# Performance work log

Hardware: AMD Instinct MI355X
Metric: run time of the kernel (lower is better)

## Reference

```python
import jax, jax.numpy as jnp
import numpy as np

N_NODES = 50000
N_EDGES = 800000
IN_DIM = 512
HEADS = 4
HID = 64
OUT = 64
NEG_SLOPE = 0.2  # DGL GATConv default


def gat_layer(x, W, attn_l, attn_r, bias, src, dst, n_nodes, heads, d_out):
    # x: [N, F_in], W: [F_in, heads*d_out], attn_l/attn_r: [heads, d_out], bias: [heads, d_out]
    f = (x @ W).reshape(n_nodes, heads, d_out)          # [N, H, D]
    el = jnp.sum(f * attn_l, axis=-1)                   # [N, H]
    er = jnp.sum(f * attn_r, axis=-1)                   # [N, H]
    e = jax.nn.leaky_relu(el[src] + er[dst], NEG_SLOPE) # [E, H]
    # segment softmax over incoming edges of each dst node
    m = jax.ops.segment_max(e, dst, num_segments=n_nodes)       # [N, H]
    ex = jnp.exp(e - m[dst])                                     # [E, H]
    den = jax.ops.segment_sum(ex, dst, num_segments=n_nodes)    # [N, H]
    a = ex / den[dst]                                            # [E, H]
    # scatter-aggregate weighted messages
    out = jax.ops.segment_sum(a[:, :, None] * f[src], dst, num_segments=n_nodes)  # [N, H, D]
    return out + bias, a


def setup_inputs() -> dict:
    key = jax.random.key(0)
    ks = jax.random.split(key, 12)
    features = jax.random.normal(ks[0], (N_NODES, IN_DIM), dtype=jnp.float32)
    src = jax.random.randint(ks[1], (N_EDGES,), 0, N_NODES, dtype=jnp.int32)
    dst = jax.random.randint(ks[2], (N_EDGES,), 0, N_NODES, dtype=jnp.int32)
    s1 = 1.0 / np.sqrt(IN_DIM)
    s2 = 1.0 / np.sqrt(HEADS * HID)
    W1 = jax.random.normal(ks[3], (IN_DIM, HEADS * HID), dtype=jnp.float32) * s1
    al1 = jax.random.normal(ks[4], (HEADS, HID), dtype=jnp.float32) * s1
    ar1 = jax.random.normal(ks[5], (HEADS, HID), dtype=jnp.float32) * s1
    b1 = jnp.zeros((HEADS, HID), dtype=jnp.float32)
    W2 = jax.random.normal(ks[6], (HEADS * HID, OUT), dtype=jnp.float32) * s2
    al2 = jax.random.normal(ks[7], (1, OUT), dtype=jnp.float32) * s2
    ar2 = jax.random.normal(ks[8], (1, OUT), dtype=jnp.float32) * s2
    b2 = jnp.zeros((1, OUT), dtype=jnp.float32)
    return {"features": features, "W1": W1, "al1": al1, "ar1": ar1, "b1": b1,
            "W2": W2, "al2": al2, "ar2": ar2, "b2": b2, "src": src, "dst": dst}


def reference(features, W1, al1, ar1, b1, W2, al2, ar2, b2, src, dst):
    h1, _ = gat_layer(features, W1, al1, ar1, b1, src, dst, N_NODES, HEADS, HID)
    h1 = jax.nn.elu(h1.reshape(N_NODES, HEADS * HID))   # flatten heads + ELU
    h2, _ = gat_layer(h1, W2, al2, ar2, b2, src, dst, N_NODES, 1, OUT)
    return h2  # [N, 1, OUT]
```

## Files before the change

kernel.cpp:

```cpp
#include <hip/hip_runtime.h>

#define N_NODES 50000
#define N_EDGES 800000
#define IN_DIM 512
#define NEG_SLOPE 0.2f

typedef short short8 __attribute__((ext_vector_type(8)));
typedef float f32x16 __attribute__((ext_vector_type(16)));
typedef __attribute__((address_space(3))) unsigned int lds_u32;
typedef const __attribute__((address_space(1))) unsigned int glb_u32;

__device__ __forceinline__ unsigned bf16rne(float f) {
  union { float f; unsigned u; } v;
  v.f = f;
  return (v.u + 0x7FFFu + ((v.u >> 16) & 1u)) >> 16;
}
__device__ __forceinline__ void tsplit8(float4 a, float4 b, short8& hi,
                                        short8& lo) {
  float fa[8] = {a.x, a.y, a.z, a.w, b.x, b.y, b.z, b.w};
#pragma unroll
  for (int i = 0; i < 8; i++) {
    unsigned u = __float_as_uint(fa[i]);
    hi[i] = (short)(u >> 16);
    float lof = fa[i] - __uint_as_float(u & 0xffff0000u);
    lo[i] = (short)(__float_as_uint(lof) >> 16);
  }
}

__global__ void pack_w(const float* __restrict__ W, short* __restrict__ Bhi,
                       int N) {
  int k = blockIdx.x, n = threadIdx.x;
  float w = W[(size_t)k * N + n];
  int ksub = k >> 4, kh = (k >> 3) & 1, j = k & 7;
  int nsub = n >> 5, lane2 = (n & 31) | (kh << 5);
  size_t off = (((size_t)ksub * (N >> 5) + nsub) * 64 + lane2) * 8 + j;
  Bhi[off] = (short)bf16rne(w);
}

template <int K, int NSUBS, int NTILES>
__global__ __launch_bounds__(256) void gemm_mfma(
    const float* __restrict__ A, const short* __restrict__ Bhi_,
    unsigned short* __restrict__ Cb, const float* __restrict__ alv,
    const float* __restrict__ arv, float2* __restrict__ elt,
    float2* __restrict__ ert, int M) {
  constexpr int N = NSUBS * 32;
  constexpr int MTILES = 4 / NTILES;
  constexpr int BROWS = MTILES * 32;
  constexpr int T = K / 32;
  constexpr int MT = MTILES;
  constexpr int GB = NSUBS / 2;
  constexpr int NSUBT = NSUBS / NTILES;
  constexpr int HPW = NSUBT / 2;
  constexpr int NHEADS = NSUBS / 2;
  constexpr int BSTEP_S = NSUBS * 1024;
  static_assert(MT + GB == 5 || MT + GB == 6, "vmcnt literal coverage");
  __shared__ float ldsA[2][BROWS * 32];
  __shared__ short ldsB[2][BSTEP_S];

  const int tid = threadIdx.x;
  const int lane = tid & 63;
  const int w = tid >> 6;
  const int l31 = lane & 31;
  const int half = lane >> 5;
  const int local_mt = w / NTILES;
  const int ntile = w % NTILES;
  const int block_row0 = blockIdx.x * BROWS;

  const float* gsrcA[MT];
#pragma unroll
  for (int q = 0; q < MT; q++) {
    int seg = w * MT + q;
    int r = seg * 8 + (lane >> 3);
    int c = (lane & 7) ^ (r & 7);
    int grow = block_row0 + r;
    if (grow > M - 1) grow = M - 1;
    gsrcA[q] = A + (size_t)grow * K + c * 4;
  }
  const short* bsrc = Bhi_ + lane * 8;

  const int arow = local_mt * 32 + l31;
  const int rs = arow & 7;

  f32x16 acc[NSUBT] = {};

  auto STAGE = [&](int b, int t) {
#pragma unroll
    for (int q = 0; q < MT; q++) {
      __builtin_amdgcn_global_load_lds((glb_u32*)(gsrcA[q] + t * 32),
                                       (lds_u32*)&ldsA[b][(w * MT + q) * 256],
                                       16, 0, 0);
    }
#pragma unroll
    for (int j = 0; j < GB; j++) {
      __builtin_amdgcn_global_load_lds(
          (glb_u32*)(bsrc + (size_t)t * BSTEP_S + (w * GB + j) * 512),
          (lds_u32*)&ldsB[b][(w * GB + j) * 512], 16, 0, 0);
    }
  };

  STAGE(0, 0);

  int buf = 0;
  for (int t = 0; t < T; t++) {
    if (t + 1 < T) {
      STAGE(buf ^ 1, t + 1);
      if constexpr (MT + GB == 5)
        asm volatile("s_waitcnt vmcnt(5)" ::: "memory");
      else
        asm volatile("s_waitcnt vmcnt(6)" ::: "memory");
    } else {
      asm volatile("s_waitcnt vmcnt(0)" ::: "memory");
    }
    __builtin_amdgcn_s_barrier();

    const float* lA = ldsA[buf];
    const short* lB = ldsB[buf];
#pragma unroll
    for (int u = 0; u < 2; u++) {
      int c0 = u * 4 + half * 2;
      float4 a0 = *(const float4*)&lA[arow * 32 + (c0 ^ rs) * 4];
      float4 a1 = *(const float4*)&lA[arow * 32 + ((c0 + 1) ^ rs) * 4];
      short8 ah, al8;
      tsplit8(a0, a1, ah, al8);
#pragma unroll
      for (int j = 0; j < NSUBT; j++) {
        short8 cbj = *(const short8*)&lB[(u * NSUBS + ntile * NSUBT + j) * 512 +
                                         lane * 8];
        acc[j] = __builtin_amdgcn_mfma_f32_32x32x16_bf16(ah, cbj, acc[j], 0, 0, 0);
        acc[j] =
            __builtin_amdgcn_mfma_f32_32x32x16_bf16(al8, cbj, acc[j], 0, 0, 0);
      }
    }
    asm volatile("s_waitcnt lgkmcnt(0)" ::: "memory");
    __builtin_amdgcn_s_barrier();
    buf ^= 1;
  }

  const int mrow0 = block_row0 + local_mt * 32;
#pragma unroll
  for (int h = 0; h < HPW; h++) {
    int c0 = ntile * NSUBT * 32 + 2 * h * 32 + l31;
    float wa0 = alv[c0], wa1 = alv[c0 + 32];
    float wr0 = arv[c0], wr1 = arv[c0 + 32];
#pragma unroll
    for (int r = 0; r < 16; r++) {
      int roff = (r & 3) + 8 * (r >> 2) + 4 * half;
      int row = mrow0 + roff;
      float v0 = acc[2 * h][r], v1 = acc[2 * h + 1][r];
      if (row < M) {
        Cb[(size_t)row * N + c0] = (unsigned short)bf16rne(v0);
        Cb[(size_t)row * N + c0 + 32] = (unsigned short)bf16rne(v1);
      }
      float elv = v0 * wa0 + v1 * wa1;
      float erv = v0 * wr0 + v1 * wr1;
#pragma unroll
      for (int off = 1; off < 32; off <<= 1) {
        elv += __shfl_xor(elv, off);
        erv += __shfl_xor(erv, off);
      }
      if (l31 == 0 && row < M) {
        int hg = ntile * HPW + h;
        elt[(size_t)row * NHEADS + hg] =
            make_float2(__expf(elv), __expf(NEG_SLOPE * elv));
        ert[(size_t)row * NHEADS + hg] =
            make_float2(__expf(erv), __expf(NEG_SLOPE * erv));
      }
    }
  }
}

__global__ void hist_kernel(const int* __restrict__ dst,
                            int* __restrict__ counts) {
  int e = blockIdx.x * blockDim.x + threadIdx.x;
  if (e < N_EDGES) atomicAdd(&counts[dst[e]], 1);
}

#define NSCAN 196
__global__ __launch_bounds__(256) void scan_part(const int* __restrict__ counts,
                                                 int* __restrict__ offsets,
                                                 int* __restrict__ bsums) {
  __shared__ int sh[256];
  int t = threadIdx.x;
  int i = blockIdx.x * 256 + t;
  int v = (i < N_NODES) ? counts[i] : 0;
  sh[t] = v;
  __syncthreads();
  for (int o = 1; o < 256; o <<= 1) {
    int x = (t >= o) ? sh[t - o] : 0;
    __syncthreads();
    sh[t] += x;
    __syncthreads();
  }
  if (i < N_NODES) offsets[i] = sh[t] - v;
  if (t == 255) bsums[blockIdx.x] = sh[255];
}
__global__ __launch_bounds__(256) void scan_top(int* __restrict__ bsums) {
  __shared__ int sh[256];
  int t = threadIdx.x;
  int v = (t < NSCAN) ? bsums[t] : 0;
  sh[t] = v;
  __syncthreads();
  for (int o = 1; o < 256; o <<= 1) {
    int x = (t >= o) ? sh[t - o] : 0;
    __syncthreads();
    sh[t] += x;
    __syncthreads();
  }
  if (t < NSCAN) bsums[t] = sh[t] - v;
}
__global__ __launch_bounds__(256) void scan_add(int* __restrict__ offsets,
                                                const int* __restrict__ bsums) {
  int i = blockIdx.x * 256 + threadIdx.x;
  if (i < N_NODES) offsets[i] += bsums[blockIdx.x];
  if (i == 0) offsets[N_NODES] = N_EDGES;
}

__global__ void scatter_kernel(const int* __restrict__ src,
                               const int* __restrict__ dst,
                               const int* __restrict__ offsets,
                               int* __restrict__ fill,
                               int* __restrict__ csr_src) {
  int e = blockIdx.x * blockDim.x + threadIdx.x;
  if (e < N_EDGES) {
    int d = dst[e];
    int pos = offsets[d] + atomicAdd(&fill[d], 1);
    csr_src[pos] = src[e];
  }
}

__global__ __launch_bounds__(256) void agg1_kernel(
    const int* __restrict__ offsets, const int* __restrict__ csr_src,
    const float2* __restrict__ elt, const float2* __restrict__ ert,
    const unsigned short* __restrict__ fb, const float* __restrict__ bias,
    float* __restrict__ h1) {
  __shared__ float red[3][256];
  __shared__ float dred[3][32];
  int n = blockIdx.x;
  int t = threadIdx.x;
  int w = t >> 6, lane = t & 63;
  int l31 = lane & 31;
  int eslot = lane >> 5;
  int h = l31 >> 3;
  int slot = w * 2 + eslot;
  int off0 = offsets[n], deg = offsets[n + 1] - off0;
  float2 fv = ert[n * 4 + h];
  float4 aLo = {0.f, 0.f, 0.f, 0.f}, aHi = {0.f, 0.f, 0.f, 0.f};
  float4 bLo = {0.f, 0.f, 0.f, 0.f}, bHi = {0.f, 0.f, 0.f, 0.f};
  float sden = 0.f;
  int i = slot;
  for (; i + 8 < deg; i += 16) {
    int s0 = csr_src[off0 + i];
    int s1 = csr_src[off0 + i + 8];
    uint4 p0 = *(const uint4*)(fb + (size_t)s0 * 256 + l31 * 8);
    uint4 p1 = *(const uint4*)(fb + (size_t)s1 * 256 + l31 * 8);
    float2 q0 = elt[s0 * 4 + h];
    float2 q1 = elt[s1 * 4 + h];
    float t10 = q0.x * fv.x, t20 = q0.y * fv.y;
    float t11 = q1.x * fv.x, t21 = q1.y * fv.y;
    float a0 = t10 > 1.f ? t10 : t20;
    float a1 = t11 > 1.f ? t11 : t21;
    sden += a0 + a1;
    aLo.x += a0 * __uint_as_float(p0.x << 16);
    aLo.y += a0 * __uint_as_float(p0.x & 0xffff0000u);
    aLo.z += a0 * __uint_as_float(p0.y << 16);
    aLo.w += a0 * __uint_as_float(p0.y & 0xffff0000u);
    aHi.x += a0 * __uint_as_float(p0.z << 16);
    aHi.y += a0 * __uint_as_float(p0.z & 0xffff0000u);
    aHi.z += a0 * __uint_as_float(p0.w << 16);
    aHi.w += a0 * __uint_as_float(p0.w & 0xffff0000u);
    bLo.x += a1 * __uint_as_float(p1.x << 16);
    bLo.y += a1 * __uint_as_float(p1.x & 0xffff0000u);
    bLo.z += a1 * __uint_as_float(p1.y << 16);
    bLo.w += a1 * __uint_as_float(p1.y & 0xffff0000u);
    bHi.x += a1 * __uint_as_float(p1.z << 16);
    bHi.y += a1 * __uint_as_float(p1.z & 0xffff0000u);
    bHi.z += a1 * __uint_as_float(p1.w << 16);
    bHi.w += a1 * __uint_as_float(p1.w & 0xffff0000u);
  }
  if (i < deg) {
    int s0 = csr_src[off0 + i];
    uint4 p0 = *(const uint4*)(fb + (size_t)s0 * 256 + l31 * 8);
    float2 q0 = elt[s0 * 4 + h];
    float t10 = q0.x * fv.x, t20 = q0.y * fv.y;
    float a0 = t10 > 1.f ? t10 : t20;
    sden += a0;
    aLo.x += a0 * __uint_as_float(p0.x << 16);
    aLo.y += a0 * __uint_as_float(p0.x & 0xffff0000u);
    aLo.z += a0 * __uint_as_float(p0.y << 16);
    aLo.w += a0 * __uint_as_float(p0.y & 0xffff0000u);
    aHi.x += a0 * __uint_as_float(p0.z << 16);
    aHi.y += a0 * __uint_as_float(p0.z & 0xffff0000u);
    aHi.z += a0 * __uint_as_float(p0.w << 16);
    aHi.w += a0 * __uint_as_float(p0.w & 0xffff0000u);
  }
  aLo.x += bLo.x; aLo.y += bLo.y; aLo.z += bLo.z; aLo.w += bLo.w;
  aHi.x += bHi.x; aHi.y += bHi.y; aHi.z += bHi.z; aHi.w += bHi.w;
  aLo.x += __shfl_xor(aLo.x, 32);
  aLo.y += __shfl_xor(aLo.y, 32);
  aLo.z += __shfl_xor(aLo.z, 32);
  aLo.w += __shfl_xor(aLo.w, 32);
  aHi.x += __shfl_xor(aHi.x, 32);
  aHi.y += __shfl_xor(aHi.y, 32);
  aHi.z += __shfl_xor(aHi.z, 32);
  aHi.w += __shfl_xor(aHi.w, 32);
  sden += __shfl_xor(sden, 32);
  if (w && lane < 32) {
    *(float4*)(&red[w - 1][l31 * 8]) = aLo;
    *(float4*)(&red[w - 1][l31 * 8 + 4]) = aHi;
    dred[w - 1][l31] = sden;
  }
  __syncthreads();
  if (w == 0 && lane < 32) {
    float den = sden;
#pragma unroll
    for (int j = 0; j < 3; j++) {
      float4 rL = *(float4*)(&red[j][l31 * 8]);
      float4 rH = *(float4*)(&red[j][l31 * 8 + 4]);
      aLo.x += rL.x; aLo.y += rL.y; aLo.z += rL.z; aLo.w += rL.w;
      aHi.x += rH.x; aHi.y += rH.y; aHi.z += rH.z; aHi.w += rH.w;
      den += dred[j][l31];
    }
    float invd = den > 0.f ? 1.0f / den : 0.f;
    float4 b0 = ((const float4*)bias)[l31 * 2];
    float4 b1 = ((const float4*)bias)[l31 * 2 + 1];
    float o[8] = {aLo.x * invd + b0.x, aLo.y * invd + b0.y,
                  aLo.z * invd + b0.z, aLo.w * invd + b0.w,
                  aHi.x * invd + b1.x, aHi.y * invd + b1.y,
                  aHi.z * invd + b1.z, aHi.w * invd + b1.w};
#pragma unroll
    for (int j = 0; j < 8; j++) o[j] = o[j] > 0.f ? o[j] : __expf(o[j]) - 1.0f;
    float4 o0 = {o[0], o[1], o[2], o[3]};
    float4 o1 = {o[4], o[5], o[6], o[7]};
    *(float4*)(h1 + (size_t)n * 256 + l31 * 8) = o0;
    *(float4*)(h1 + (size_t)n * 256 + l31 * 8 + 4) = o1;
  }
}

__global__ __launch_bounds__(256) void agg2_kernel(
    const int* __restrict__ offsets, const int* __restrict__ csr_src,
    const float2* __restrict__ elt, const float2* __restrict__ ert,
    const unsigned short* __restrict__ fb2, const float* __restrict__ bias,
    float* __restrict__ out) {
  int w = threadIdx.x >> 6, lane = threadIdx.x & 63;
  int n = blockIdx.x * 4 + w;
  if (n >= N_NODES) return;
  int dg = lane & 15, eslot = lane >> 4;
  int off0 = offsets[n], deg = offsets[n + 1] - off0;
  float2 fv = ert[n];
  float4 acc = {0.f, 0.f, 0.f, 0.f};
  float4 acc2 = {0.f, 0.f, 0.f, 0.f};
  float sden = 0.f;
  int i = eslot;
  for (; i + 4 < deg; i += 8) {
    int s0 = csr_src[off0 + i];
    int s1 = csr_src[off0 + i + 4];
    uint2 p0 = *(const uint2*)(fb2 + (size_t)s0 * 64 + dg * 4);
    uint2 p1 = *(const uint2*)(fb2 + (size_t)s1 * 64 + dg * 4);
    float2 q0 = elt[s0];
    float2 q1 = elt[s1];
    float t10 = q0.x * fv.x, t20 = q0.y * fv.y;
    float t11 = q1.x * fv.x, t21 = q1.y * fv.y;
    float a0 = t10 > 1.f ? t10 : t20;
    float a1 = t11 > 1.f ? t11 : t21;
    sden += a0 + a1;
    acc.x += a0 * __uint_as_float(p0.x << 16);
    acc.y += a0 * __uint_as_float(p0.x & 0xffff0000u);
    acc.z += a0 * __uint_as_float(p0.y << 16);
    acc.w += a0 * __uint_as_float(p0.y & 0xffff0000u);
    acc2.x += a1 * __uint_as_float(p1.x << 16);
    acc2.y += a1 * __uint_as_float(p1.x & 0xffff0000u);
    acc2.z += a1 * __uint_as_float(p1.y << 16);
    acc2.w += a1 * __uint_as_float(p1.y & 0xffff0000u);
  }
  if (i < deg) {
    int s0 = csr_src[off0 + i];
    uint2 p0 = *(const uint2*)(fb2 + (size_t)s0 * 64 + dg * 4);
    float2 q0 = elt[s0];
    float t10 = q0.x * fv.x, t20 = q0.y * fv.y;
    float a0 = t10 > 1.f ? t10 : t20;
    sden += a0;
    acc.x += a0 * __uint_as_float(p0.x << 16);
    acc.y += a0 * __uint_as_float(p0.x & 0xffff0000u);
    acc.z += a0 * __uint_as_float(p0.y << 16);
    acc.w += a0 * __uint_as_float(p0.y & 0xffff0000u);
  }
  acc.x += acc2.x;
  acc.y += acc2.y;
  acc.z += acc2.z;
  acc.w += acc2.w;
#pragma unroll
  for (int off = 16; off < 64; off <<= 1) {
    acc.x += __shfl_xor(acc.x, off);
    acc.y += __shfl_xor(acc.y, off);
    acc.z += __shfl_xor(acc.z, off);
    acc.w += __shfl_xor(acc.w, off);
    sden += __shfl_xor(sden, off);
  }
  if (eslot == 0) {
    float invd = sden > 0.f ? 1.0f / sden : 0.f;
    float4 b = ((const float4*)bias)[dg];
    float4 ov = {acc.x * invd + b.x, acc.y * invd + b.y, acc.z * invd + b.z,
                 acc.w * invd + b.w};
    *(float4*)(out + (size_t)n * 64 + dg * 4) = ov;
  }
}

extern "C" void kernel_launch(void* const* d_in, const int* in_sizes, int n_in,
                              void* d_out, int out_size, void* d_ws,
                              size_t ws_size, hipStream_t stream) {
  const float* features = (const float*)d_in[0];
  const float* W1 = (const float*)d_in[1];
  const float* al1 = (const float*)d_in[2];
  const float* ar1 = (const float*)d_in[3];
  const float* b1 = (const float*)d_in[4];
  const float* W2 = (const float*)d_in[5];
  const float* al2 = (const float*)d_in[6];
  const float* ar2 = (const float*)d_in[7];
  const float* b2 = (const float*)d_in[8];
  const int* src = (const int*)d_in[9];
  const int* dst = (const int*)d_in[10];
  float* out = (float*)d_out;

  float* h1 = (float*)d_ws;
  unsigned short* fb = (unsigned short*)(h1 + (size_t)N_NODES * 256);
  unsigned short* fb2 = fb;
  float2* elt1 = (float2*)(fb + (size_t)N_NODES * 256);
  float2* ert1 = elt1 + (size_t)N_NODES * 4;
  float2* elt2 = ert1 + (size_t)N_NODES * 4;
  float2* ert2 = elt2 + N_NODES;
  int* counts = (int*)(ert2 + N_NODES);
  int* offsets = counts + N_NODES;
  int* fill = offsets + N_NODES + 1;
  int* csr_src = fill + N_NODES;
  int* bsums = csr_src + N_EDGES;

  short* b1hi = (short*)d_out;
  short* b2hi = (short*)fill;

  hipMemsetAsync(counts, 0, N_NODES * sizeof(int), stream);
  hipMemsetAsync(fill, 0, N_NODES * sizeof(int), stream);
  hist_kernel<<<(N_EDGES + 255) / 256, 256, 0, stream>>>(dst, counts);
  scan_part<<<NSCAN, 256, 0, stream>>>(counts, offsets, bsums);
  scan_top<<<1, 256, 0, stream>>>(bsums);
  scan_add<<<NSCAN, 256, 0, stream>>>(offsets, bsums);
  scatter_kernel<<<(N_EDGES + 255) / 256, 256, 0, stream>>>(src, dst, offsets,
                                                            fill, csr_src);

  pack_w<<<512, 256, 0, stream>>>(W1, b1hi, 256);
  pack_w<<<256, 64, 0, stream>>>(W2, b2hi, 64);

  gemm_mfma<IN_DIM, 8, 2><<<782, 256, 0, stream>>>(features, b1hi, fb, al1,
                                                   ar1, elt1, ert1, N_NODES);
  agg1_kernel<<<N_NODES, 256, 0, stream>>>(offsets, csr_src, elt1, ert1, fb,
                                           b1, h1);

  gemm_mfma<256, 2, 1><<<391, 256, 0, stream>>>(h1, b2hi, fb2, al2, ar2, elt2,
                                                ert2, N_NODES);
  agg2_kernel<<<(N_NODES + 3) / 4, 256, 0, stream>>>(offsets, csr_src, elt2,
                                                     ert2, fb2, b2, out);
}
```

Baseline: 417.9 us.

## Map one wave per node in layer-1 aggregation and retile first GEMM

The layer-1 aggregation kernel now gives each destination node a single wave instead of a full 256-thread block. Each lane owns four of the 256 features and walks all incoming edges, unrolled by four with two accumulator sets. This removes the LDS cross-wave reduction and the block barrier, and launches four nodes per block. The first GEMM switches to NTILES=4, giving 32-row blocks with twice as many blocks, and the vmcnt wait is fixed to 5 loads per step. The trade-off is a serial edge loop per wave, which makes high-degree nodes slower, and narrower 8-byte gathers per lane.

```diff
diff --git a/kernel.cpp b/kernel.cpp
--- a/kernel.cpp
+++ b/kernel.cpp
@@ -53,7 +53,7 @@
   constexpr int HPW = NSUBT / 2;
   constexpr int NHEADS = NSUBS / 2;
   constexpr int BSTEP_S = NSUBS * 1024;
-  static_assert(MT + GB == 5 || MT + GB == 6, "vmcnt literal coverage");
+  static_assert(MT + GB == 5, "vmcnt literal assumes 5 loads/wave/step");
   __shared__ float ldsA[2][BROWS * 32];
   __shared__ short ldsB[2][BSTEP_S];
 
@@ -104,10 +104,7 @@
   for (int t = 0; t < T; t++) {
     if (t + 1 < T) {
       STAGE(buf ^ 1, t + 1);
-      if constexpr (MT + GB == 5)
-        asm volatile("s_waitcnt vmcnt(5)" ::: "memory");
-      else
-        asm volatile("s_waitcnt vmcnt(6)" ::: "memory");
+      asm volatile("s_waitcnt vmcnt(5)" ::: "memory");
     } else {
       asm volatile("s_waitcnt vmcnt(0)" ::: "memory");
     }
@@ -233,107 +230,82 @@
     const float2* __restrict__ elt, const float2* __restrict__ ert,
     const unsigned short* __restrict__ fb, const float* __restrict__ bias,
     float* __restrict__ h1) {
-  __shared__ float red[3][256];
-  __shared__ float dred[3][32];
-  int n = blockIdx.x;
-  int t = threadIdx.x;
-  int w = t >> 6, lane = t & 63;
-  int l31 = lane & 31;
-  int eslot = lane >> 5;
-  int h = l31 >> 3;
-  int slot = w * 2 + eslot;
+  int w = threadIdx.x >> 6, lane = threadIdx.x & 63;
+  int n = blockIdx.x * 4 + w;
+  if (n >= N_NODES) return;
+  int h = lane >> 4;
   int off0 = offsets[n], deg = offsets[n + 1] - off0;
   float2 fv = ert[n * 4 + h];
-  float4 aLo = {0.f, 0.f, 0.f, 0.f}, aHi = {0.f, 0.f, 0.f, 0.f};
-  float4 bLo = {0.f, 0.f, 0.f, 0.f}, bHi = {0.f, 0.f, 0.f, 0.f};
-  float sden = 0.f;
-  int i = slot;
-  for (; i + 8 < deg; i += 16) {
+  float4 acc = {0.f, 0.f, 0.f, 0.f};
+  float4 acc2 = {0.f, 0.f, 0.f, 0.f};
+  float sden = 0.f, sden2 = 0.f;
+  const unsigned short* fbl = fb + lane * 4;
+  int i = 0;
+  for (; i + 3 < deg; i += 4) {
     int s0 = csr_src[off0 + i];
-    int s1 = csr_src[off0 + i + 8];
-    uint4 p0 = *(const uint4*)(fb + (size_t)s0 * 256 + l31 * 8);
-    uint4 p1 = *(const uint4*)(fb + (size_t)s1 * 256 + l31 * 8);
+    int s1 = csr_src[off0 + i + 1];
+    int s2 = csr_src[off0 + i + 2];
+    int s3 = csr_src[off0 + i + 3];
+    uint2 p0 = *(const uint2*)(fbl + (size_t)s0 * 256);
+    uint2 p1 = *(const uint2*)(fbl + (size_t)s1 * 256);
+    uint2 p2 = *(const uint2*)(fbl + (size_t)s2 * 256);
+    uint2 p3 = *(const uint2*)(fbl + (size_t)s3 * 256);
     float2 q0 = elt[s0 * 4 + h];
     float2 q1 = elt[s1 * 4 + h];
-    float t10 = q0.x * fv.x, t20 = q0.y * fv.y;
-    float t11 = q1.x * fv.x, t21 = q1.y * fv.y;
-    float a0 = t10 > 1.f ? t10 : t20;
-    float a1 = t11 > 1.f ? t11 : t21;
-    sden += a0 + a1;
-    aLo.x += a0 * __uint_as_float(p0.x << 16);
-    aLo.y += a0 * __uint_as_float(p0.x & 0xffff0000u);
-    aLo.z += a0 * __uint_as_float(p0.y << 16);
-    aLo.w += a0 * __uint_as_float(p0.y & 0xffff0000u);
-    aHi.x += a0 * __uint_as_float(p0.z << 16);
-    aHi.y += a0 * __uint_as_float(p0.z & 0xffff0000u);
-    aHi.z += a0 * __uint_as_float(p0.w << 16);
-    aHi.w += a0 * __uint_as_float(p0.w & 0xffff0000u);
-    bLo.x += a1 * __uint_as_float(p1.x << 16);
-    bLo.y += a1 * __uint_as_float(p1.x & 0xffff0000u);
-    bLo.z += a1 * __uint_as_float(p1.y << 16);
-    bLo.w += a1 * __uint_as_float(p1.y & 0xffff0000u);
-    bHi.x += a1 * __uint_as_float(p1.z << 16);
-    bHi.y += a1 * __uint_as_float(p1.z & 0xffff0000u);
-    bHi.z += a1 * __uint_as_float(p1.w << 16);
-    bHi.w += a1 * __uint_as_float(p1.w & 0xffff0000u);
-  }
-  if (i < deg) {
+    float2 q2 = elt[s2 * 4 + h];
+    float2 q3 = elt[s3 * 4 + h];
+    float t0 = q0.x * fv.x, u0 = q0.y * fv.y;
+    float t1 = q1.x * fv.x, u1 = q1.y * fv.y;
+    float t2 = q2.x * fv.x, u2 = q2.y * fv.y;
+    float t3 = q3.x * fv.x, u3 = q3.y * fv.y;
+    float a0 = t0 > 1.f ? t0 : u0;
+    float a1 = t1 > 1.f ? t1 : u1;
+    float a2 = t2 > 1.f ? t2 : u2;
+    float a3 = t3 > 1.f ? t3 : u3;
+    sden += a0 + a2;
+    sden2 += a1 + a3;
+    acc.x += a0 * __uint_as_float(p0.x << 16);
+    acc.y += a0 * __uint_as_float(p0.x & 0xffff0000u);
+    acc.z += a0 * __uint_as_float(p0.y << 16);
+    acc.w += a0 * __uint_as_float(p0.y & 0xffff0000u);
+    acc2.x += a1 * __uint_as_float(p1.x << 16);
+    acc2.y += a1 * __uint_as_float(p1.x & 0xffff0000u);
+    acc2.z += a1 * __uint_as_float(p1.y << 16);
+    acc2.w += a1 * __uint_as_float(p1.y & 0xffff0000u);
+    acc.x += a2 * __uint_as_float(p2.x << 16);
+    acc.y += a2 * __uint_as_float(p2.x & 0xffff0000u);
+    acc.z += a2 * __uint_as_float(p2.y << 16);
+    acc.w += a2 * __uint_as_float(p2.y & 0xffff0000u);
+    acc2.x += a3 * __uint_as_float(p3.x << 16);
+    acc2.y += a3 * __uint_as_float(p3.x & 0xffff0000u);
+    acc2.z += a3 * __uint_as_float(p3.y << 16);
+    acc2.w += a3 * __uint_as_float(p3.y & 0xffff0000u);
+  }
+  for (; i < deg; i++) {
     int s0 = csr_src[off0 + i];
-    uint4 p0 = *(const uint4*)(fb + (size_t)s0 * 256 + l31 * 8);
+    uint2 p0 = *(const uint2*)(fbl + (size_t)s0 * 256);
     float2 q0 = elt[s0 * 4 + h];
-    float t10 = q0.x * fv.x, t20 = q0.y * fv.y;
-    float a0 = t10 > 1.f ? t10 : t20;
+    float t0 = q0.x * fv.x, u0 = q0.y * fv.y;
+    float a0 = t0 > 1.f ? t0 : u0;
     sden += a0;
-    aLo.x += a0 * __uint_as_float(p0.x << 16);
-    aLo.y += a0 * __uint_as_float(p0.x & 0xffff0000u);
-    aLo.z += a0 * __uint_as_float(p0.y << 16);
-    aLo.w += a0 * __uint_as_float(p0.y & 0xffff0000u);
-    aHi.x += a0 * __uint_as_float(p0.z << 16);
-    aHi.y += a0 * __uint_as_float(p0.z & 0xffff0000u);
-    aHi.z += a0 * __uint_as_float(p0.w << 16);
-    aHi.w += a0 * __uint_as_float(p0.w & 0xffff0000u);
-  }
-  aLo.x += bLo.x; aLo.y += bLo.y; aLo.z += bLo.z; aLo.w += bLo.w;
-  aHi.x += bHi.x; aHi.y += bHi.y; aHi.z += bHi.z; aHi.w += bHi.w;
-  aLo.x += __shfl_xor(aLo.x, 32);
-  aLo.y += __shfl_xor(aLo.y, 32);
-  aLo.z += __shfl_xor(aLo.z, 32);
-  aLo.w += __shfl_xor(aLo.w, 32);
-  aHi.x += __shfl_xor(aHi.x, 32);
-  aHi.y += __shfl_xor(aHi.y, 32);
-  aHi.z += __shfl_xor(aHi.z, 32);
-  aHi.w += __shfl_xor(aHi.w, 32);
-  sden += __shfl_xor(sden, 32);
-  if (w && lane < 32) {
-    *(float4*)(&red[w - 1][l31 * 8]) = aLo;
-    *(float4*)(&red[w - 1][l31 * 8 + 4]) = aHi;
-    dred[w - 1][l31] = sden;
-  }
-  __syncthreads();
-  if (w == 0 && lane < 32) {
-    float den = sden;
-#pragma unroll
-    for (int j = 0; j < 3; j++) {
-      float4 rL = *(float4*)(&red[j][l31 * 8]);
-      float4 rH = *(float4*)(&red[j][l31 * 8 + 4]);
-      aLo.x += rL.x; aLo.y += rL.y; aLo.z += rL.z; aLo.w += rL.w;
-      aHi.x += rH.x; aHi.y += rH.y; aHi.z += rH.z; aHi.w += rH.w;
-      den += dred[j][l31];
-    }
-    float invd = den > 0.f ? 1.0f / den : 0.f;
-    float4 b0 = ((const float4*)bias)[l31 * 2];
-    float4 b1 = ((const float4*)bias)[l31 * 2 + 1];
-    float o[8] = {aLo.x * invd + b0.x, aLo.y * invd + b0.y,
-                  aLo.z * invd + b0.z, aLo.w * invd + b0.w,
-                  aHi.x * invd + b1.x, aHi.y * invd + b1.y,
-                  aHi.z * invd + b1.z, aHi.w * invd + b1.w};
-#pragma unroll
-    for (int j = 0; j < 8; j++) o[j] = o[j] > 0.f ? o[j] : __expf(o[j]) - 1.0f;
-    float4 o0 = {o[0], o[1], o[2], o[3]};
-    float4 o1 = {o[4], o[5], o[6], o[7]};
-    *(float4*)(h1 + (size_t)n * 256 + l31 * 8) = o0;
-    *(float4*)(h1 + (size_t)n * 256 + l31 * 8 + 4) = o1;
-  }
+    acc.x += a0 * __uint_as_float(p0.x << 16);
+    acc.y += a0 * __uint_as_float(p0.x & 0xffff0000u);
+    acc.z += a0 * __uint_as_float(p0.y << 16);
+    acc.w += a0 * __uint_as_float(p0.y & 0xffff0000u);
+  }
+  acc.x += acc2.x;
+  acc.y += acc2.y;
+  acc.z += acc2.z;
+  acc.w += acc2.w;
+  sden += sden2;
+  float invd = sden > 0.f ? 1.0f / sden : 0.f;
+  float4 b = ((const float4*)bias)[lane];
+  float o[4] = {acc.x * invd + b.x, acc.y * invd + b.y, acc.z * invd + b.z,
+                acc.w * invd + b.w};
+#pragma unroll
+  for (int j = 0; j < 4; j++) o[j] = o[j] > 0.f ? o[j] : __expf(o[j]) - 1.0f;
+  float4 ov = {o[0], o[1], o[2], o[3]};
+  *(float4*)(h1 + (size_t)n * 256 + lane * 4) = ov;
 }
 
 __global__ __launch_bounds__(256) void agg2_kernel(
@@ -449,10 +421,10 @@
   pack_w<<<512, 256, 0, stream>>>(W1, b1hi, 256);
   pack_w<<<256, 64, 0, stream>>>(W2, b2hi, 64);
 
-  gemm_mfma<IN_DIM, 8, 2><<<782, 256, 0, stream>>>(features, b1hi, fb, al1,
-                                                   ar1, elt1, ert1, N_NODES);
-  agg1_kernel<<<N_NODES, 256, 0, stream>>>(offsets, csr_src, elt1, ert1, fb,
-                                           b1, h1);
+  gemm_mfma<IN_DIM, 8, 4><<<1563, 256, 0, stream>>>(features, b1hi, fb, al1,
+                                                    ar1, elt1, ert1, N_NODES);
+  agg1_kernel<<<(N_NODES + 3) / 4, 256, 0, stream>>>(offsets, csr_src, elt1,
+                                                     ert1, fb, b1, h1);
 
   gemm_mfma<256, 2, 1><<<391, 256, 0, stream>>>(h1, b2hi, fb2, al2, ar2, elt2,
                                                 ert2, N_NODES);
```

After: 408.5 us. -2.3%, faster.
